# Optimization experiments

Hardware: AMD Instinct MI355X
Metric: run time of the kernel (lower is better)

Reference implementation:

```python
import math
import jax, jax.numpy as jnp
import numpy as np

B, S, E = 4, 2048, 1024

def setup_inputs() -> dict:
    key = jax.random.key(0)
    k1, k2, k3 = jax.random.split(key, 3)
    X = jax.random.normal(k1, (B, S, E), dtype=jnp.float32)
    # nn.Linear(E, 3E): weight [3E, E], bias [3E]; scale weights for sane softmax
    W = jax.random.normal(k2, (3 * E, E), dtype=jnp.float32) * (1.0 / math.sqrt(E))
    b = jax.random.normal(k3, (3 * E,), dtype=jnp.float32) * 0.01
    return {"X": X, "W": W, "b": b}

def reference(X, W, b):
    E_ = X.shape[-1]
    # fused QKV projection: X @ W^T + b -> [B, S, 3E]
    qkv = jnp.einsum('bse,fe->bsf', X, W) + b
    q, k, v = jnp.split(qkv, 3, axis=-1)
    scores = jnp.einsum('bqe,bke->bqk', q, k) / math.sqrt(E_)
    attention_weight = jax.nn.softmax(scores, axis=-1)  # [B, S, S]
    output = jnp.einsum('bqk,bke->bqe', attention_weight, v)
    return (output, attention_weight)
```

## Files before the change

kernel.cpp:

```cpp
#include <hip/hip_runtime.h>
#include <math.h>

typedef __bf16 bf16;
typedef __bf16 bf16x4 __attribute__((ext_vector_type(4)));
typedef __bf16 bf16x8 __attribute__((ext_vector_type(8)));
typedef float f32x4 __attribute__((ext_vector_type(4)));

__device__ inline void gload_lds16(const bf16* g, bf16* l) {
    __builtin_amdgcn_global_load_lds(
        (const __attribute__((address_space(1))) void*)g,
        (__attribute__((address_space(3))) void*)l, 16, 0, 0);
}

template <typename OutT, bool HAS_BIAS>
__global__ __launch_bounds__(256) void mfma_nt(
    const bf16* __restrict__ A, const bf16* __restrict__ B,
    const float* __restrict__ bias, OutT* __restrict__ C,
    int K, int lda, int ldb, int ldc,
    long sA, long sB, long sC, float alpha)
{
    A += (long)blockIdx.z * sA;
    B += (long)blockIdx.z * sB;
    C += (long)blockIdx.z * sC;

    __shared__ bf16 As[128 * 32] __attribute__((aligned(16)));
    __shared__ bf16 Bs[128 * 32] __attribute__((aligned(16)));

    const int t  = threadIdx.x;
    const int m0 = blockIdx.y * 128;
    const int n0 = blockIdx.x * 128;

    const int lane = t & 63;
    const int wave = t >> 6;
    const int wrow = (wave >> 1) * 64;
    const int wcol = (wave & 1) * 64;
    const int fr   = lane & 15;
    const int kq   = (lane >> 4) * 8;

    const int r0 = t >> 2,           k80 = (t & 3) * 8;
    const int r1 = (t + 256) >> 2,   k81 = ((t + 256) & 3) * 8;

    f32x4 acc[4][4] = {};

    for (int k0 = 0; k0 < K; k0 += 32) {
        gload_lds16(A + (long)(m0 + r0) * lda + k0 + k80, &As[t * 8]);
        gload_lds16(A + (long)(m0 + r1) * lda + k0 + k81, &As[(t + 256) * 8]);
        gload_lds16(B + (long)(n0 + r0) * ldb + k0 + k80, &Bs[t * 8]);
        gload_lds16(B + (long)(n0 + r1) * ldb + k0 + k81, &Bs[(t + 256) * 8]);
        __syncthreads();

        bf16x8 af[4], bfr[4];
#pragma unroll
        for (int i = 0; i < 4; i++) {
            af[i]  = *(const bf16x8*)&As[(wrow + i * 16 + fr) * 32 + kq];
            bfr[i] = *(const bf16x8*)&Bs[(wcol + i * 16 + fr) * 32 + kq];
        }
#pragma unroll
        for (int i = 0; i < 4; i++)
#pragma unroll
            for (int j = 0; j < 4; j++)
                acc[i][j] = __builtin_amdgcn_mfma_f32_16x16x32_bf16(
                    af[i], bfr[j], acc[i][j], 0, 0, 0);
        __syncthreads();
    }

    const int r4 = (lane >> 4) * 4;
#pragma unroll
    for (int j = 0; j < 4; j++) {
        const int col = n0 + wcol + j * 16 + fr;
        const float bv = HAS_BIAS ? bias[col] : 0.f;
#pragma unroll
        for (int i = 0; i < 4; i++) {
#pragma unroll
            for (int r = 0; r < 4; r++) {
                const long row = m0 + wrow + i * 16 + r4 + r;
                float v = alpha * acc[i][j][r] + bv;
                C[row * ldc + col] = (OutT)v;
            }
        }
    }
}

__global__ __launch_bounds__(256) void f32_to_bf16(
    const float* __restrict__ in, bf16* __restrict__ out, long n)
{
    long i = ((long)blockIdx.x * 256 + threadIdx.x) * 4;
    if (i < n) {
        float4 v = *(const float4*)(in + i);
        bf16x4 o = { (bf16)v.x, (bf16)v.y, (bf16)v.z, (bf16)v.w };
        *(bf16x4*)(out + i) = o;
    }
}

__global__ __launch_bounds__(256) void transpose_v(
    const bf16* __restrict__ V, bf16* __restrict__ Vt)
{
    __shared__ bf16 tile[32][33];
    const bf16* Vb  = V  + (long)blockIdx.z * 2048 * 3072;
    bf16*       Vtb = Vt + (long)blockIdx.z * 1024 * 2048;
    const int s0 = blockIdx.x * 32, e0 = blockIdx.y * 32;
    const int tx = threadIdx.x & 31, ty = threadIdx.x >> 5;
#pragma unroll
    for (int i = 0; i < 32; i += 8)
        tile[ty + i][tx] = Vb[(long)(s0 + ty + i) * 3072 + e0 + tx];
    __syncthreads();
#pragma unroll
    for (int i = 0; i < 32; i += 8)
        Vtb[(long)(e0 + ty + i) * 2048 + s0 + tx] = tile[tx][ty + i];
}

__global__ __launch_bounds__(256) void softmax_rows(
    float* __restrict__ P, bf16* __restrict__ Pb)
{
    float* row = P + (long)blockIdx.x * 2048;
    bf16* prow = Pb + (long)blockIdx.x * 2048;
    const int t = threadIdx.x;
    float4 v0 = *(const float4*)(row + t * 4);
    float4 v1 = *(const float4*)(row + (t + 256) * 4);

    float m = fmaxf(fmaxf(fmaxf(v0.x, v0.y), fmaxf(v0.z, v0.w)),
                    fmaxf(fmaxf(v1.x, v1.y), fmaxf(v1.z, v1.w)));
#pragma unroll
    for (int o = 32; o > 0; o >>= 1) m = fmaxf(m, __shfl_xor(m, o));

    __shared__ float red[4];
    const int wid = t >> 6, lane = t & 63;
    if (lane == 0) red[wid] = m;
    __syncthreads();
    m = fmaxf(fmaxf(red[0], red[1]), fmaxf(red[2], red[3]));
    __syncthreads();

    v0.x = __expf(v0.x - m); v0.y = __expf(v0.y - m);
    v0.z = __expf(v0.z - m); v0.w = __expf(v0.w - m);
    v1.x = __expf(v1.x - m); v1.y = __expf(v1.y - m);
    v1.z = __expf(v1.z - m); v1.w = __expf(v1.w - m);

    float s = (v0.x + v0.y + v0.z + v0.w) + (v1.x + v1.y + v1.z + v1.w);
#pragma unroll
    for (int o = 32; o > 0; o >>= 1) s += __shfl_xor(s, o);
    if (lane == 0) red[wid] = s;
    __syncthreads();
    s = red[0] + red[1] + red[2] + red[3];

    const float inv = 1.0f / s;
    v0.x *= inv; v0.y *= inv; v0.z *= inv; v0.w *= inv;
    v1.x *= inv; v1.y *= inv; v1.z *= inv; v1.w *= inv;
    *(float4*)(row + t * 4) = v0;
    *(float4*)(row + (t + 256) * 4) = v1;
    bf16x4 p0 = { (bf16)v0.x, (bf16)v0.y, (bf16)v0.z, (bf16)v0.w };
    bf16x4 p1 = { (bf16)v1.x, (bf16)v1.y, (bf16)v1.z, (bf16)v1.w };
    *(bf16x4*)(prow + t * 4) = p0;
    *(bf16x4*)(prow + (t + 256) * 4) = p1;
}

extern "C" void kernel_launch(void* const* d_in, const int* in_sizes, int n_in,
                              void* d_out, int out_size, void* d_ws, size_t ws_size,
                              hipStream_t stream)
{
    const int B = 4, S = 2048, E = 1024;
    const float* X    = (const float*)d_in[0];
    const float* W    = (const float*)d_in[1];
    const float* bias = (const float*)d_in[2];

    float* out0 = (float*)d_out;
    float* out1 = out0 + (long)B * S * E;

    char* ws = (char*)d_ws;
    bf16* qkvb = (bf16*)(ws);
    bf16* Vt   = (bf16*)(ws + 50331648);
    bf16* Pb   = (bf16*)(ws + 67108864);
    bf16* Xb   = (bf16*)(ws + 67108864);
    bf16* Wb   = (bf16*)(ws + 67108864 + 16777216);

    f32_to_bf16<<<(long)B * S * E / 1024, 256, 0, stream>>>(X, Xb, (long)B * S * E);
    f32_to_bf16<<<(long)3 * E * E / 1024, 256, 0, stream>>>(W, Wb, (long)3 * E * E);

    mfma_nt<bf16, true><<<dim3(3 * E / 128, B * S / 128, 1), 256, 0, stream>>>(
        Xb, Wb, bias, qkvb, E, E, E, 3 * E, 0, 0, 0, 1.0f);

    mfma_nt<float, false><<<dim3(S / 128, S / 128, B), 256, 0, stream>>>(
        qkvb, qkvb + E, nullptr, out1, E, 3 * E, 3 * E, S,
        (long)S * 3 * E, (long)S * 3 * E, (long)S * S, 0.03125f);

    transpose_v<<<dim3(S / 32, E / 32, B), 256, 0, stream>>>(qkvb + 2 * E, Vt);

    softmax_rows<<<B * S, 256, 0, stream>>>(out1, Pb);

    mfma_nt<float, false><<<dim3(E / 128, S / 128, B), 256, 0, stream>>>(
        Pb, Vt, nullptr, out0, S, S, S, E,
        (long)S * S, (long)E * S, (long)S * E, 1.0f);
}
```

Before: 352.1 us.

## Fuse softmax exp and row sums into score GEMM, transpose V in QKV epilogue

```diff
diff --git a/kernel.cpp b/kernel.cpp
--- a/kernel.cpp
+++ b/kernel.cpp
@@ -6,22 +6,28 @@
 typedef __bf16 bf16x8 __attribute__((ext_vector_type(8)));
 typedef float f32x4 __attribute__((ext_vector_type(4)));
 
+#define MODE_QKV    0
+#define MODE_SCORES 1
+#define MODE_PV     2
+
 __device__ inline void gload_lds16(const bf16* g, bf16* l) {
     __builtin_amdgcn_global_load_lds(
         (const __attribute__((address_space(1))) void*)g,
         (__attribute__((address_space(3))) void*)l, 16, 0, 0);
 }
 
-template <typename OutT, bool HAS_BIAS>
+template <int MODE>
 __global__ __launch_bounds__(256) void mfma_nt(
     const bf16* __restrict__ A, const bf16* __restrict__ B,
-    const float* __restrict__ bias, OutT* __restrict__ C,
+    const float* __restrict__ bias, void* __restrict__ Cv,
+    bf16* __restrict__ Vt, float* __restrict__ lsum,
     int K, int lda, int ldb, int ldc,
     long sA, long sB, long sC, float alpha)
 {
     A += (long)blockIdx.z * sA;
     B += (long)blockIdx.z * sB;
-    C += (long)blockIdx.z * sC;
+    char* Cb = (char*)Cv + (long)blockIdx.z * sC;
+    if constexpr (MODE != MODE_QKV) lsum += (long)blockIdx.z * 2048;
 
     __shared__ bf16 As[128 * 32] __attribute__((aligned(16)));
     __shared__ bf16 Bs[128 * 32] __attribute__((aligned(16)));
@@ -65,18 +71,91 @@
     }
 
     const int r4 = (lane >> 4) * 4;
-#pragma unroll
-    for (int j = 0; j < 4; j++) {
-        const int col = n0 + wcol + j * 16 + fr;
-        const float bv = HAS_BIAS ? bias[col] : 0.f;
-#pragma unroll
-        for (int i = 0; i < 4; i++) {
-#pragma unroll
-            for (int r = 0; r < 4; r++) {
-                const long row = m0 + wrow + i * 16 + r4 + r;
-                float v = alpha * acc[i][j][r] + bv;
-                C[row * ldc + col] = (OutT)v;
+
+    if constexpr (MODE == MODE_QKV) {
+        if (n0 >= 2048) {
+#pragma unroll
+            for (int j = 0; j < 4; j++) {
+                const int col = n0 + wcol + j * 16 + fr;
+                const float bv = bias[col];
+                const int e = col - 2048;
+#pragma unroll
+                for (int i = 0; i < 4; i++) {
+                    const int row = m0 + wrow + i * 16 + r4;
+                    const int b = row >> 11, s = row & 2047;
+                    bf16x4 pk;
+#pragma unroll
+                    for (int r = 0; r < 4; r++) pk[r] = (bf16)(acc[i][j][r] + bv);
+                    *(bf16x4*)(Vt + ((long)b * 1024 + e) * 2048 + s) = pk;
+                }
             }
+        } else {
+            bf16* C = (bf16*)Cb;
+#pragma unroll
+            for (int j = 0; j < 4; j++) {
+                const int col = n0 + wcol + j * 16 + fr;
+                const float bv = bias[col];
+#pragma unroll
+                for (int i = 0; i < 4; i++)
+#pragma unroll
+                    for (int r = 0; r < 4; r++) {
+                        const long row = m0 + wrow + i * 16 + r4 + r;
+                        C[row * ldc + col] = (bf16)(acc[i][j][r] + bv);
+                    }
+            }
+        }
+    } else if constexpr (MODE == MODE_SCORES) {
+        bf16* C = (bf16*)Cb;
+        float rsum[4][4];
+#pragma unroll
+        for (int i = 0; i < 4; i++)
+#pragma unroll
+            for (int r = 0; r < 4; r++) rsum[i][r] = 0.f;
+#pragma unroll
+        for (int j = 0; j < 4; j++) {
+            const int col = n0 + wcol + j * 16 + fr;
+#pragma unroll
+            for (int i = 0; i < 4; i++)
+#pragma unroll
+                for (int r = 0; r < 4; r++) {
+                    const long row = m0 + wrow + i * 16 + r4 + r;
+                    const float e = __expf(alpha * acc[i][j][r]);
+                    C[row * ldc + col] = (bf16)e;
+                    rsum[i][r] += e;
+                }
+        }
+#pragma unroll
+        for (int off = 1; off < 16; off <<= 1)
+#pragma unroll
+            for (int i = 0; i < 4; i++)
+#pragma unroll
+                for (int r = 0; r < 4; r++)
+                    rsum[i][r] += __shfl_xor(rsum[i][r], off);
+        if (fr == 0) {
+#pragma unroll
+            for (int i = 0; i < 4; i++)
+#pragma unroll
+                for (int r = 0; r < 4; r++)
+                    atomicAdd(&lsum[m0 + wrow + i * 16 + r4 + r], rsum[i][r]);
+        }
+    } else {
+        float* C = (float*)Cb;
+        float linv[4][4];
+#pragma unroll
+        for (int i = 0; i < 4; i++)
+#pragma unroll
+            for (int r = 0; r < 4; r++)
+                linv[i][r] = 1.0f / lsum[m0 + wrow + i * 16 + r4 + r];
+#pragma unroll
+        for (int j = 0; j < 4; j++) {
+            const int col = n0 + wcol + j * 16 + fr;
+#pragma unroll
+            for (int i = 0; i < 4; i++)
+#pragma unroll
+                for (int r = 0; r < 4; r++) {
+                    const long row = m0 + wrow + i * 16 + r4 + r;
+                    C[row * ldc + col] = acc[i][j][r] * linv[i][r];
+                }
         }
     }
 }
@@ -92,65 +171,23 @@
     }
 }
 
-__global__ __launch_bounds__(256) void transpose_v(
-    const bf16* __restrict__ V, bf16* __restrict__ Vt)
-{
-    __shared__ bf16 tile[32][33];
-    const bf16* Vb  = V  + (long)blockIdx.z * 2048 * 3072;
-    bf16*       Vtb = Vt + (long)blockIdx.z * 1024 * 2048;
-    const int s0 = blockIdx.x * 32, e0 = blockIdx.y * 32;
-    const int tx = threadIdx.x & 31, ty = threadIdx.x >> 5;
-#pragma unroll
-    for (int i = 0; i < 32; i += 8)
-        tile[ty + i][tx] = Vb[(long)(s0 + ty + i) * 3072 + e0 + tx];
-    __syncthreads();
-#pragma unroll
-    for (int i = 0; i < 32; i += 8)
-        Vtb[(long)(e0 + ty + i) * 2048 + s0 + tx] = tile[tx][ty + i];
-}
-
-__global__ __launch_bounds__(256) void softmax_rows(
-    float* __restrict__ P, bf16* __restrict__ Pb)
-{
-    float* row = P + (long)blockIdx.x * 2048;
-    bf16* prow = Pb + (long)blockIdx.x * 2048;
+__global__ __launch_bounds__(256) void normalize_rows(
+    const bf16* __restrict__ Pu, const float* __restrict__ l,
+    float* __restrict__ out1)
+{
+    const long row = blockIdx.x;
+    const float inv = 1.0f / l[row];
+    const bf16* p = Pu + row * 2048;
+    float* o = out1 + row * 2048;
     const int t = threadIdx.x;
-    float4 v0 = *(const float4*)(row + t * 4);
-    float4 v1 = *(const float4*)(row + (t + 256) * 4);
-
-    float m = fmaxf(fmaxf(fmaxf(v0.x, v0.y), fmaxf(v0.z, v0.w)),
-                    fmaxf(fmaxf(v1.x, v1.y), fmaxf(v1.z, v1.w)));
-#pragma unroll
-    for (int o = 32; o > 0; o >>= 1) m = fmaxf(m, __shfl_xor(m, o));
-
-    __shared__ float red[4];
-    const int wid = t >> 6, lane = t & 63;
-    if (lane == 0) red[wid] = m;
-    __syncthreads();
-    m = fmaxf(fmaxf(red[0], red[1]), fmaxf(red[2], red[3]));
-    __syncthreads();
-
-    v0.x = __expf(v0.x - m); v0.y = __expf(v0.y - m);
-    v0.z = __expf(v0.z - m); v0.w = __expf(v0.w - m);
-    v1.x = __expf(v1.x - m); v1.y = __expf(v1.y - m);
-    v1.z = __expf(v1.z - m); v1.w = __expf(v1.w - m);
-
-    float s = (v0.x + v0.y + v0.z + v0.w) + (v1.x + v1.y + v1.z + v1.w);
-#pragma unroll
-    for (int o = 32; o > 0; o >>= 1) s += __shfl_xor(s, o);
-    if (lane == 0) red[wid] = s;
-    __syncthreads();
-    s = red[0] + red[1] + red[2] + red[3];
-
-    const float inv = 1.0f / s;
-    v0.x *= inv; v0.y *= inv; v0.z *= inv; v0.w *= inv;
-    v1.x *= inv; v1.y *= inv; v1.z *= inv; v1.w *= inv;
-    *(float4*)(row + t * 4) = v0;
-    *(float4*)(row + (t + 256) * 4) = v1;
-    bf16x4 p0 = { (bf16)v0.x, (bf16)v0.y, (bf16)v0.z, (bf16)v0.w };
-    bf16x4 p1 = { (bf16)v1.x, (bf16)v1.y, (bf16)v1.z, (bf16)v1.w };
-    *(bf16x4*)(prow + t * 4) = p0;
-    *(bf16x4*)(prow + (t + 256) * 4) = p1;
+    bf16x8 v = *(const bf16x8*)(p + t * 8);
+    float4 a, b;
+    a.x = (float)v[0] * inv; a.y = (float)v[1] * inv;
+    a.z = (float)v[2] * inv; a.w = (float)v[3] * inv;
+    b.x = (float)v[4] * inv; b.y = (float)v[5] * inv;
+    b.z = (float)v[6] * inv; b.w = (float)v[7] * inv;
+    *(float4*)(o + t * 8)     = a;
+    *(float4*)(o + t * 8 + 4) = b;
 }
 
 extern "C" void kernel_launch(void* const* d_in, const int* in_sizes, int n_in,
@@ -166,27 +203,30 @@
     float* out1 = out0 + (long)B * S * E;
 
     char* ws = (char*)d_ws;
-    bf16* qkvb = (bf16*)(ws);
-    bf16* Vt   = (bf16*)(ws + 50331648);
-    bf16* Pb   = (bf16*)(ws + 67108864);
-    bf16* Xb   = (bf16*)(ws + 67108864);
-    bf16* Wb   = (bf16*)(ws + 67108864 + 16777216);
+    bf16* QKb = (bf16*)(ws);
+    bf16* Vt  = (bf16*)(ws + 33554432);
+    bf16* Pu  = (bf16*)(ws + 50331648);
+    float* l  = (float*)(ws + 83886080);
+    bf16* Xb  = (bf16*)(ws + 50331648);
+    bf16* Wb  = (bf16*)(ws + 67108864);
 
     f32_to_bf16<<<(long)B * S * E / 1024, 256, 0, stream>>>(X, Xb, (long)B * S * E);
     f32_to_bf16<<<(long)3 * E * E / 1024, 256, 0, stream>>>(W, Wb, (long)3 * E * E);
-
-    mfma_nt<bf16, true><<<dim3(3 * E / 128, B * S / 128, 1), 256, 0, stream>>>(
-        Xb, Wb, bias, qkvb, E, E, E, 3 * E, 0, 0, 0, 1.0f);
-
-    mfma_nt<float, false><<<dim3(S / 128, S / 128, B), 256, 0, stream>>>(
-        qkvb, qkvb + E, nullptr, out1, E, 3 * E, 3 * E, S,
-        (long)S * 3 * E, (long)S * 3 * E, (long)S * S, 0.03125f);
-
-    transpose_v<<<dim3(S / 32, E / 32, B), 256, 0, stream>>>(qkvb + 2 * E, Vt);
-
-    softmax_rows<<<B * S, 256, 0, stream>>>(out1, Pb);
-
-    mfma_nt<float, false><<<dim3(E / 128, S / 128, B), 256, 0, stream>>>(
-        Pb, Vt, nullptr, out0, S, S, S, E,
-        (long)S * S, (long)E * S, (long)S * E, 1.0f);
-}
+    hipMemsetAsync(l, 0, (long)B * S * sizeof(float), stream);
+
+    mfma_nt<MODE_QKV><<<dim3(3 * E / 128, B * S / 128, 1), 256, 0, stream>>>(
+        Xb, Wb, bias, QKb, Vt, nullptr,
+        E, E, E, 2048, 0, 0, 0, 1.0f);
+
+    mfma_nt<MODE_SCORES><<<dim3(S / 128, S / 128, B), 256, 0, stream>>>(
+        QKb, QKb + 1024, nullptr, Pu, nullptr, l,
+        E, 2048, 2048, S,
+        (long)S * 2048, (long)S * 2048, (long)S * S * 2 , 0.03125f);
+
+    normalize_rows<<<B * S, 256, 0, stream>>>(Pu, l, out1);
+
+    mfma_nt<MODE_PV><<<dim3(E / 128, S / 128, B), 256, 0, stream>>>(
+        Pu, Vt, nullptr, out0, nullptr, l,
+        S, S, S, E,
+        (long)S * S, (long)E * S, (long)S * E * 4 , 1.0f);
+}
```

New measurement: 358.9 us. Within noise of the previous version (+1.9%).
